# Performance work log

Measured on AMD Instinct MI355X. Metric: run time of the kernel, lower is better.

Reference implementation:

```python
import jax, jax.numpy as jnp
import numpy as np

N_NODES = 50000
N_EDGES = 600000
F_IN = 128
H = 128
NUM_GRAPHS = 64
SELF_LOOP_W = 2.0  # improved=True


def setup_inputs() -> dict:
    key = jax.random.key(0)
    ks = jax.random.split(key, 16)
    x = jax.random.normal(ks[0], (N_NODES, F_IN), dtype=jnp.float32)
    edge_index = jax.random.randint(ks[1], (2, N_EDGES), 0, N_NODES, dtype=jnp.int64)
    batch_index = jnp.sort(jax.random.randint(ks[2], (N_NODES,), 0, NUM_GRAPHS, dtype=jnp.int64))
    edge_weight = jax.random.uniform(ks[3], (N_EDGES,), dtype=jnp.float32)
    def lin(k, fin, fout):
        s = 1.0 / np.sqrt(fin)
        kw, kb = jax.random.split(k)
        W = jax.random.uniform(kw, (fin, fout), minval=-s, maxval=s, dtype=jnp.float32)
        b = jax.random.uniform(kb, (fout,), minval=-s, maxval=s, dtype=jnp.float32)
        return W, b
    W0, b0 = lin(ks[4], F_IN, H)
    W1, b1 = lin(ks[5], H, H)
    W2, b2 = lin(ks[6], H, H)
    W3, b3 = lin(ks[7], H, H)
    Wout, bout = lin(ks[8], 2 * H, 1)
    return dict(x=x, edge_index=edge_index, batch_index=batch_index, edge_weight=edge_weight,
                W0=W0, b0=b0, W1=W1, b1=b1, W2=W2, b2=b2, W3=W3, b3=b3, Wout=Wout, bout=bout)


def reference(x, edge_index, batch_index, edge_weight, W0, b0, W1, b1, W2, b2, W3, b3, Wout, bout):
    N = x.shape[0]
    loop = jnp.arange(N)
    src = jnp.concatenate([edge_index[0], loop])  # [E+N]
    dst = jnp.concatenate([edge_index[1], loop])
    w = jnp.concatenate([edge_weight, jnp.full((N,), SELF_LOOP_W, dtype=x.dtype)])
    # symmetric GCN normalization: deg over destination, norm = d^-1/2[src]*w*d^-1/2[dst]
    deg = jax.ops.segment_sum(w, dst, num_segments=N)
    dinv = jnp.where(deg > 0, jax.lax.rsqrt(deg), 0.0)
    norm = dinv[src] * w * dinv[dst]  # [E+N]

    def conv(h, W, b):
        h = h @ W  # dense transform before aggregation
        msg = h[src] * norm[:, None]
        return jax.ops.segment_sum(msg, dst, num_segments=N) + b

    h = jnp.tanh(conv(x, W0, b0))
    h = jnp.tanh(conv(h, W1, b1))
    h = jnp.tanh(conv(h, W2, b2))
    h = jnp.tanh(conv(h, W3, b3))

    gmax = jax.ops.segment_max(h, batch_index, num_segments=NUM_GRAPHS)
    gmax = jnp.where(jnp.isfinite(gmax), gmax, 0.0)  # guard empty graphs
    cnt = jax.ops.segment_sum(jnp.ones((N,), dtype=h.dtype), batch_index, num_segments=NUM_GRAPHS)
    gmean = jax.ops.segment_sum(h, batch_index, num_segments=NUM_GRAPHS) / jnp.maximum(cnt, 1.0)[:, None]
    hidden = jnp.concatenate([gmax, gmean], axis=1)  # [B, 2H]
    out = hidden @ Wout + bout  # [B, 1]
    return out, hidden
```

## Files before the change

### kernel.cpp

```cpp
#include <hip/hip_runtime.h>
#include <hip/hip_bf16.h>
#include <hip/hip_fp16.h>

typedef __hip_bfloat16 bf16;
typedef _Float16 half8 __attribute__((ext_vector_type(8)));
typedef float f32x4 __attribute__((ext_vector_type(4)));

#define FDIM 128
#define SELF_W 2.0f
#define NGRAPH 64
#define DEG_SCALE 1048576.0f
#define DEG_MASK  ((1ull<<44) - 1ull)

__device__ __forceinline__ float b2f(bf16 v){ return __bfloat162float(v); }

__device__ __forceinline__ float rdf(const void* p, long long i, int f32){
  return f32 ? ((const float*)p)[i] : b2f(((const bf16*)p)[i]);
}
__device__ __forceinline__ int rdi(const void* p, long long i, int i64){
  return i64 ? (int)(((const long long*)p)[i]) : ((const int*)p)[i];
}

__device__ __forceinline__ float tanh_fast(float x){
  float ax = fabsf(x);
  float e  = __expf(-2.0f*ax);
  float r  = (1.0f - e) * __builtin_amdgcn_rcpf(1.0f + e);
  return copysignf(r, x);
}

struct PtrPack { const void* p[10]; };
__global__ __launch_bounds__(256) void k_setup(PtrPack pk, float* __restrict__ pf,
                                               _Float16* __restrict__ wt,
                                               unsigned long long* __restrict__ packed,
                                               const void* __restrict__ bat,
                                               unsigned* __restrict__ gstart,
                                               const unsigned short* __restrict__ x16,
                                               const int* __restrict__ ei32,
                                               int* __restrict__ flags_out,
                                               int N){
  __shared__ int cbig, codd, sf32, si64;
  int tid = threadIdx.x;
  if (tid == 0){ cbig = 0; codd = 0; }
  __syncthreads();
  for (int i = tid; i < 4096; i += 256){
    int e = (x16[i] >> 7) & 0xFF;
    if (e >= 134) atomicAdd(&cbig, 1);
  }
  for (int i = tid; i < 512; i += 256){
    if (ei32[2*i + 1] != 0) atomicAdd(&codd, 1);
  }
  __syncthreads();
  if (tid == 0){
    sf32 = (cbig >= 64) ? 1 : 0;
    si64 = (codd < 8)  ? 1 : 0;
    if (blockIdx.x == 0){ flags_out[0] = sf32; flags_out[1] = si64; }
  }
  __syncthreads();
  int f32 = sf32, i64 = si64;

  const int sz[10]  = {16384,16384,16384,16384,128,128,128,128,256,1};
  const int dst[10] = {0,16384,32768,49152,65536,65664,65792,65920,66048,66304};
  int i = blockIdx.x*blockDim.x + tid;
  if (i < 66305){
    int seg = 0, rem = i;
    while (rem >= sz[seg]){ rem -= sz[seg]; seg++; }
    float v = rdf(pk.p[seg], rem, f32);
    pf[dst[seg] + rem] = v;
    if (seg < 4){
      int k = rem >> 7, n = rem & 127;
      wt[seg*16384 + n*128 + k] = (_Float16)v;
    }
  }
  int stride = gridDim.x*blockDim.x;
  for (int j = i; j < N; j += stride)
    packed[j] = (unsigned long long)(SELF_W * DEG_SCALE);
  if (blockIdx.x == gridDim.x - 1){
    __shared__ unsigned s[NGRAPH+1];
    int g = tid;
    if (g <= NGRAPH){
      int lo = 0, hi = N;
      while (lo < hi){ int mid = (lo + hi) >> 1; if (rdi(bat, mid, i64) < g) lo = mid + 1; else hi = mid; }
      s[g] = (unsigned)lo;
    }
    __syncthreads();
    if (g <= NGRAPH) gstart[g] = s[g];
  }
}

__global__ void k_edge_deg(const void* __restrict__ ei, const void* __restrict__ ew,
                           unsigned long long* __restrict__ packed,
                           unsigned* __restrict__ rank,
                           int E, int N, const int* __restrict__ flags){
  int e0 = 2*(blockIdx.x*blockDim.x + threadIdx.x);
  if (e0 >= E) return;
  int i64 = flags[1], f32 = flags[0];
  int e1 = e0 + 1;
  bool h1 = (e1 < E);
  int d0 = rdi(ei, (long long)E + e0, i64);
  int d1 = h1 ? rdi(ei, (long long)E + e1, i64) : 0;
  float w0 = rdf(ew, e0, f32);
  float w1 = h1 ? rdf(ew, e1, f32) : 0.f;
  unsigned r0 = 0u, r1 = 0u;
  if ((unsigned)d0 < (unsigned)N){
    unsigned long long add = (1ull << 44) |
        (unsigned long long)__float2uint_rn(w0 * DEG_SCALE);
    r0 = (unsigned)(atomicAdd(&packed[d0], add) >> 44);
  }
  if (h1 && (unsigned)d1 < (unsigned)N){
    unsigned long long add = (1ull << 44) |
        (unsigned long long)__float2uint_rn(w1 * DEG_SCALE);
    r1 = (unsigned)(atomicAdd(&packed[d1], add) >> 44);
  }
  rank[e0] = r0;
  if (h1) rank[e1] = r1;
}

__device__ __forceinline__ unsigned wave_incl_scan(unsigned v){
  int lane = threadIdx.x & 63;
  #pragma unroll
  for (int d = 1; d < 64; d <<= 1){
    unsigned t = __shfl_up(v, d, 64);
    if (lane >= d) v += t;
  }
  return v;
}

__global__ __launch_bounds__(256) void k_scan_pre(const unsigned long long* __restrict__ packed,
                                                  float* __restrict__ dinv,
                                                  float* __restrict__ swv,
                                                  unsigned* __restrict__ bsum,
                                                  unsigned* __restrict__ epk, unsigned Epad,
                                                  int N){
  __shared__ unsigned wsh[4];
  int tid = threadIdx.x, lane = tid & 63, wid = tid >> 6;
  unsigned gid = blockIdx.x*blockDim.x + tid, gstr = gridDim.x*blockDim.x;
  for (unsigned j = gid; j < Epad; j += gstr) epk[j] = 0u;
  int i0 = blockIdx.x*1024 + tid*4;
  unsigned tsum = 0u;
  #pragma unroll
  for (int j = 0; j < 4; j++){
    int i = i0 + j;
    if (i < N){
      unsigned long long pv = packed[i];
      tsum += ((unsigned)(pv >> 44) + 7u) & ~7u;
      float d = (float)(pv & DEG_MASK) * (1.0f / DEG_SCALE);
      float di = (d > 0.f) ? rsqrtf(d) : 0.f;
      dinv[i] = di;
      swv[i]  = di * di * SELF_W;
    }
  }
  #pragma unroll
  for (int d = 1; d < 64; d <<= 1) tsum += __shfl_down(tsum, d, 64);
  if (lane == 0) wsh[wid] = tsum;
  __syncthreads();
  if (tid == 0) bsum[blockIdx.x] = wsh[0] + wsh[1] + wsh[2] + wsh[3];
}

__global__ __launch_bounds__(256) void k_scan_fin(const unsigned long long* __restrict__ packed,
                                                  const unsigned* __restrict__ bsum,
                                                  unsigned* __restrict__ off, int N, int NB){
  __shared__ unsigned wsh[4];
  __shared__ unsigned sbase, stot;
  int tid = threadIdx.x, lane = tid & 63, wid = tid >> 6;
  if (tid < 64){
    unsigned v = (tid < NB) ? bsum[tid] : 0u;
    unsigned isc = wave_incl_scan(v);
    if (tid == (int)blockIdx.x) sbase = isc - v;
    if (tid == 63) stot = isc;
  }
  __syncthreads();
  int i0 = blockIdx.x*1024 + tid*4;
  unsigned v0=0u,v1=0u,v2=0u,v3=0u;
  if (i0+0 < N) v0 = ((unsigned)(packed[i0+0] >> 44) + 7u) & ~7u;
  if (i0+1 < N) v1 = ((unsigned)(packed[i0+1] >> 44) + 7u) & ~7u;
  if (i0+2 < N) v2 = ((unsigned)(packed[i0+2] >> 44) + 7u) & ~7u;
  if (i0+3 < N) v3 = ((unsigned)(packed[i0+3] >> 44) + 7u) & ~7u;
  unsigned tsum = v0+v1+v2+v3;
  unsigned isc = wave_incl_scan(tsum);
  if (lane == 63) wsh[wid] = isc;
  __syncthreads();
  unsigned wbase = 0u;
  #pragma unroll
  for (int w = 0; w < 4; w++) if (w < wid) wbase += wsh[w];
  unsigned ex = sbase + wbase + (isc - tsum);
  if (i0+0 < N) off[i0+0] = ex;
  if (i0+1 < N) off[i0+1] = ex + v0;
  if (i0+2 < N) off[i0+2] = ex + v0 + v1;
  if (i0+3 < N) off[i0+3] = ex + v0 + v1 + v2;
  if (blockIdx.x == gridDim.x - 1 && tid == 0) off[N] = stot;
}

__global__ void k_bucket(const void* __restrict__ ei, const void* __restrict__ ew,
                         const float* __restrict__ dinv,
                         const unsigned* __restrict__ off,
                         const unsigned* __restrict__ rank,
                         unsigned* __restrict__ epk,
                         int E, unsigned Epad, int N, const int* __restrict__ flags){
  int e0 = 2*(blockIdx.x*blockDim.x + threadIdx.x);
  if (e0 >= E) return;
  int i64 = flags[1], f32 = flags[0];
  #pragma unroll
  for (int j = 0; j < 2; j++){
    int e = e0 + j;
    if (e >= E) break;
    int s_ = rdi(ei, e, i64);
    int d  = rdi(ei, (long long)E + e, i64);
    if ((unsigned)s_ >= (unsigned)N || (unsigned)d >= (unsigned)N) continue;
    unsigned pos = off[d] + rank[e];
    if (pos < Epad){
      float coef = dinv[s_] * rdf(ew, e, f32) * dinv[d];
      _Float16 ch = (_Float16)coef;
      unsigned cu = (unsigned)__builtin_bit_cast(unsigned short, ch);
      epk[pos] = ((unsigned)s_ & 0xffffu) | (cu << 16);
    }
  }
}

template<int MODE>
__global__ __launch_bounds__(256) void k_gemm(const void* __restrict__ in,
                                              const _Float16* __restrict__ WT,
                                              _Float16* __restrict__ outp, int N,
                                              size_t pstride,
                                              const int* __restrict__ flags){
  __shared__ _Float16 sout[4*16*136];
  int tid  = threadIdx.x;
  int wid  = tid >> 6, lane = tid & 63;
  int ln   = lane & 15, quad = lane >> 4;
  int row0 = blockIdx.x * 64;
  int rowA = row0 + wid*16 + ln;
  int rA   = (rowA < N) ? rowA : (N > 0 ? N-1 : 0);

  half8 af[4];
  if (MODE == 1){
    const _Float16* src = (const _Float16*)in;
    #pragma unroll
    for (int kc = 0; kc < 4; kc++)
      af[kc] = *(const half8*)(src + (size_t)kc*pstride + (size_t)rA*32 + quad*8);
  } else {
    if (flags[0]){
      const float* src = (const float*)in + (size_t)rA*FDIM + quad*8;
      #pragma unroll
      for (int kc = 0; kc < 4; kc++){
        float4 a = *(const float4*)(src + kc*32);
        float4 b = *(const float4*)(src + kc*32 + 4);
        half8 h; h[0]=(_Float16)a.x; h[1]=(_Float16)a.y; h[2]=(_Float16)a.z; h[3]=(_Float16)a.w;
        h[4]=(_Float16)b.x; h[5]=(_Float16)b.y; h[6]=(_Float16)b.z; h[7]=(_Float16)b.w;
        af[kc] = h;
      }
    } else {
      const unsigned short* src = (const unsigned short*)in + (size_t)rA*FDIM + quad*8;
      #pragma unroll
      for (int kc = 0; kc < 4; kc++){
        ushort4 u0 = *(const ushort4*)(src + kc*32);
        ushort4 u1 = *(const ushort4*)(src + kc*32 + 4);
        half8 h;
        h[0]=(_Float16)__uint_as_float((unsigned)u0.x<<16);
        h[1]=(_Float16)__uint_as_float((unsigned)u0.y<<16);
        h[2]=(_Float16)__uint_as_float((unsigned)u0.z<<16);
        h[3]=(_Float16)__uint_as_float((unsigned)u0.w<<16);
        h[4]=(_Float16)__uint_as_float((unsigned)u1.x<<16);
        h[5]=(_Float16)__uint_as_float((unsigned)u1.y<<16);
        h[6]=(_Float16)__uint_as_float((unsigned)u1.z<<16);
        h[7]=(_Float16)__uint_as_float((unsigned)u1.w<<16);
        af[kc] = h;
      }
    }
  }

  f32x4 acc[8];
  #pragma unroll
  for (int nt = 0; nt < 8; nt++) acc[nt] = (f32x4){0.f,0.f,0.f,0.f};

  #pragma unroll
  for (int kc = 0; kc < 4; kc++){
    #pragma unroll
    for (int nt = 0; nt < 8; nt++){
      half8 bf = *(const half8*)(WT + (size_t)(nt*16 + ln)*FDIM + kc*32 + quad*8);
      acc[nt] = __builtin_amdgcn_mfma_f32_16x16x32_f16(af[kc], bf, acc[nt], 0, 0, 0);
    }
  }

  _Float16* so = sout + wid*2176;
  #pragma unroll
  for (int nt = 0; nt < 8; nt++)
    #pragma unroll
    for (int reg = 0; reg < 4; reg++)
      so[(quad*4 + reg)*136 + nt*16 + ln] = (_Float16)acc[nt][reg];
  __syncthreads();

  #pragma unroll
  for (int c = 0; c < 4; c++){
    int chunk = tid + c*256;
    int r = chunk >> 4, co = (chunk & 15)*8;
    int row = row0 + r;
    if (row < N){
      half8 v = *(const half8*)(sout + (r>>4)*2176 + (r&15)*136 + co);
      *(half8*)(outp + (size_t)(co>>5)*pstride + (size_t)row*32 + (co & 31)) = v;
    }
  }
}

__global__ __launch_bounds__(256) void k_agg(const _Float16* __restrict__ tp,
                                             const float* __restrict__ swv,
                                             const unsigned* __restrict__ off,
                                             const unsigned* __restrict__ epk,
                                             const float* __restrict__ bias,
                                             _Float16* __restrict__ hp,
                                             int N, size_t pstride){
  int tid  = threadIdx.x;
  int wv   = tid >> 6, lane = tid & 63;
  int quad = lane >> 4, ql = lane & 15;
  int panel = blockIdx.x & 3;
  int n = (blockIdx.x >> 2)*16 + wv*4 + quad;
  bool valid = (n < N);
  int nn = valid ? n : 0;
  const _Float16* tpp = tp + (size_t)panel*pstride;
  const _Float16* myt = tpp + ql*2;

  float sw = swv[nn];
  float2 sv = __half22float2(*(const __half2*)(myt + (size_t)nn*32));
  float a0 = sw * sv.x, a1 = sw * sv.y;
  float b0 = 0.f, b1 = 0.f;

  unsigned beg = off[nn];
  unsigned end = valid ? off[nn+1] : beg;
  if (beg < end){
    uint4 p0 = *(const uint4*)(epk + beg);
    uint4 p1 = *(const uint4*)(epk + beg + 4);
    for (unsigned i = beg; i < end; i += 8){
      unsigned ni  = i + 8;
      unsigned pre = (ni < end) ? ni : beg;
      uint4 q0 = *(const uint4*)(epk + pre);
      uint4 q1 = *(const uint4*)(epk + pre + 4);
      unsigned vs[8] = {p0.x,p0.y,p0.z,p0.w,p1.x,p1.y,p1.z,p1.w};
      __half2 tv[8];
      #pragma unroll
      for (int j = 0; j < 8; j++)
        tv[j] = *(const __half2*)(myt + (size_t)(vs[j] & 0xffffu)*32);
      #pragma unroll
      for (int j = 0; j < 8; j++){
        float w = (float)__builtin_bit_cast(_Float16, (unsigned short)(vs[j] >> 16));
        float2 tf = __half22float2(tv[j]);
        if (j & 1){ b0 += w * tf.x; b1 += w * tf.y; }
        else      { a0 += w * tf.x; a1 += w * tf.y; }
      }
      p0 = q0; p1 = q1;
    }
  }
  a0 += b0; a1 += b1;
  int cc = panel*32 + ql*2;
  a0 = tanh_fast(a0 + bias[cc]);
  a1 = tanh_fast(a1 + bias[cc+1]);
  if (valid)
    *(__half2*)(hp + (size_t)panel*pstride + (size_t)n*32 + ql*2) = __floats2half2_rn(a0, a1);
}

__global__ __launch_bounds__(256) void k_pool_part(const _Float16* __restrict__ hp,
                                                   const unsigned* __restrict__ gstart,
                                                   float* __restrict__ pmax,
                                                   float* __restrict__ psum,
                                                   size_t pstride){
  int g = blockIdx.x >> 4, sub = blockIdx.x & 15;
  int tid = threadIdx.x;
  int col = tid & 127, half_ = tid >> 7;
  const _Float16* hpp = hp + (size_t)(col >> 5)*pstride + (col & 31);
  unsigned s0 = gstart[g], s1 = gstart[g+1];
  float m = -INFINITY, sm = 0.f;
  for (unsigned n = s0 + sub*2 + half_; n < s1; n += 32){
    float v = (float)hpp[(size_t)n*32];
    m = fmaxf(m, v); sm += v;
  }
  __shared__ float shm[256], shs[256];
  shm[tid] = m; shs[tid] = sm;
  __syncthreads();
  if (half_ == 0){
    m  = fmaxf(m, shm[tid + 128]);
    sm += shs[tid + 128];
    int slot = (g*16 + sub)*128 + col;
    pmax[slot] = m;
    psum[slot] = sm;
  }
}

__global__ __launch_bounds__(256) void k_pool_out(const float* __restrict__ pmax,
                                                  const float* __restrict__ psum,
                                                  const unsigned* __restrict__ gstart,
                                                  const float* __restrict__ Wout,
                                                  const float* __restrict__ bout,
                                                  void* __restrict__ outp,
                                                  const int* __restrict__ flags){
  int g = blockIdx.x, tid = threadIdx.x;
  int col = tid & 127, sub = tid >> 7;
  unsigned cnt = gstart[g+1] - gstart[g];
  float val;
  if (sub == 0){
    float m = -INFINITY;
    #pragma unroll
    for (int j = 0; j < 16; j++) m = fmaxf(m, pmax[(g*16 + j)*128 + col]);
    val = (cnt > 0 && m > -INFINITY) ? m : 0.f;
  } else {
    float s = 0.f;
    #pragma unroll
    for (int j = 0; j < 16; j++) s += psum[(g*16 + j)*128 + col];
    val = s / (float)(cnt ? cnt : 1u);
  }
  int hcol = sub*128 + col;
  int f32out = flags[0];
  int hidx = NGRAPH + g*(2*FDIM) + hcol;
  if (f32out) ((float*)outp)[hidx] = val;
  else        ((bf16*)outp)[hidx] = __float2bfloat16(val);

  __shared__ float red[256];
  red[hcol] = val * Wout[hcol];
  __syncthreads();
  for (int s = 128; s > 0; s >>= 1){
    if (tid < s) red[tid] += red[tid + s];
    __syncthreads();
  }
  if (tid == 0){
    float o = red[0] + bout[0];
    if (f32out) ((float*)outp)[g] = o;
    else        ((bf16*)outp)[g] = __float2bfloat16(o);
  }
}

extern "C" void kernel_launch(void* const* d_in, const int* in_sizes, int n_in,
                              void* d_out, int out_size, void* d_ws, size_t ws_size,
                              hipStream_t stream){
  int N = in_sizes[0] / FDIM;
  int E = in_sizes[3];
  int NB = (N + 1023) / 1024;
  unsigned Epad = (unsigned)E + 8u*(unsigned)N;
  size_t pstride = (size_t)N * 32;

  char* p = (char*)d_ws;
  auto alloc = [&](size_t bytes){ char* r = p; p += (bytes + 255) & ~(size_t)255; return r; };
  int*       flags  = (int*)      alloc(16);
  float*     pf     = (float*)    alloc((size_t)(66305 + 64)*4);
  _Float16*  wt     = (_Float16*) alloc((size_t)4*FDIM*FDIM*2);
  unsigned long long* packed = (unsigned long long*)alloc((size_t)N*8);
  float*     dinv   = (float*)    alloc((size_t)N*4);
  float*     swv    = (float*)    alloc((size_t)N*4);
  unsigned*  off    = (unsigned*) alloc((size_t)(N+1)*4);
  unsigned*  bsum   = (unsigned*) alloc((size_t)128*4);
  unsigned*  rank   = (unsigned*) alloc((size_t)E*4);
  unsigned*  epk    = (unsigned*) alloc((size_t)Epad*4);
  _Float16*  th     = (_Float16*) alloc((size_t)N*FDIM*2);
  _Float16*  hh     = (_Float16*) alloc((size_t)N*FDIM*2);
  float*     pmax   = (float*)    alloc((size_t)NGRAPH*16*128*4);
  float*     psum   = (float*)    alloc((size_t)NGRAPH*16*128*4);
  unsigned*  gstart = (unsigned*) alloc((size_t)(NGRAPH+1)*4);

  float* bf_[4] = {pf + 65536, pf + 65664, pf + 65792, pf + 65920};
  float* Woutf  = pf + 66048;
  float* boutf  = pf + 66304;

  PtrPack pk;
  pk.p[0]=d_in[4]; pk.p[1]=d_in[6]; pk.p[2]=d_in[8]; pk.p[3]=d_in[10];
  pk.p[4]=d_in[5]; pk.p[5]=d_in[7]; pk.p[6]=d_in[9]; pk.p[7]=d_in[11];
  pk.p[8]=d_in[12]; pk.p[9]=d_in[13];
  k_setup<<<(66305 + 255)/256, 256, 0, stream>>>(pk, pf, wt, packed, d_in[2], gstart,
                                                 (const unsigned short*)d_in[0],
                                                 (const int*)d_in[1], flags, N);
  int gE2 = (E + 511)/512;
  k_edge_deg<<<gE2, 256, 0, stream>>>(d_in[1], d_in[3], packed, rank, E, N, flags);
  k_scan_pre<<<NB, 256, 0, stream>>>(packed, dinv, swv, bsum, epk, Epad, N);
  k_scan_fin<<<NB, 256, 0, stream>>>(packed, bsum, off, N, NB);
  k_bucket<<<gE2, 256, 0, stream>>>(d_in[1], d_in[3], dinv, off, rank, epk, E, Epad, N, flags);

  int gG = (N + 63)/64;
  int gA = ((N + 15)/16)*4;

  k_gemm<0><<<gG, 256, 0, stream>>>(d_in[0], wt + 0*16384, th, N, pstride, flags);
  k_agg<<<gA, 256, 0, stream>>>(th, swv, off, epk, bf_[0], hh, N, pstride);
  for (int l = 1; l < 4; l++){
    k_gemm<1><<<gG, 256, 0, stream>>>(hh, wt + (size_t)l*16384, th, N, pstride, flags);
    k_agg<<<gA, 256, 0, stream>>>(th, swv, off, epk, bf_[l], hh, N, pstride);
  }

  k_pool_part<<<16*NGRAPH, 256, 0, stream>>>(hh, gstart, pmax, psum, pstride);
  k_pool_out<<<NGRAPH, 256, 0, stream>>>(pmax, psum, gstart, Woutf, boutf, d_out, flags);
}
```

Measured before the change: 368.1 us.

## Fuse all stages into one persistent cooperative kernel with grid barriers

Replaces the chain of roughly thirteen separate kernel launches (setup, degree, scan, bucket, four GEMM/aggregate layers, pooling) with a single persistent cooperative kernel. Stages are separated by a software grid barrier built on an atomic counter. Blocks loop over tiles and vertex blocks with a grid-stride pattern, capped at 512 blocks or the occupancy limit. This removes launch gaps and the flags round-trip through memory. In exchange it pays one grid-wide barrier per stage, limits parallelism to the resident block count, and adds an extra memset launch for the barrier counter.

```diff
diff --git a/kernel.cpp b/kernel.cpp
--- a/kernel.cpp
+++ b/kernel.cpp
@@ -9,6 +9,7 @@
 #define FDIM 128
 #define SELF_W 2.0f
 #define NGRAPH 64
+#define GBMAX 512
 #define DEG_SCALE 1048576.0f
 #define DEG_MASK  ((1ull<<44) - 1ull)
 
@@ -26,93 +27,6 @@
   float e  = __expf(-2.0f*ax);
   float r  = (1.0f - e) * __builtin_amdgcn_rcpf(1.0f + e);
   return copysignf(r, x);
-}
-
-struct PtrPack { const void* p[10]; };
-__global__ __launch_bounds__(256) void k_setup(PtrPack pk, float* __restrict__ pf,
-                                               _Float16* __restrict__ wt,
-                                               unsigned long long* __restrict__ packed,
-                                               const void* __restrict__ bat,
-                                               unsigned* __restrict__ gstart,
-                                               const unsigned short* __restrict__ x16,
-                                               const int* __restrict__ ei32,
-                                               int* __restrict__ flags_out,
-                                               int N){
-  __shared__ int cbig, codd, sf32, si64;
-  int tid = threadIdx.x;
-  if (tid == 0){ cbig = 0; codd = 0; }
-  __syncthreads();
-  for (int i = tid; i < 4096; i += 256){
-    int e = (x16[i] >> 7) & 0xFF;
-    if (e >= 134) atomicAdd(&cbig, 1);
-  }
-  for (int i = tid; i < 512; i += 256){
-    if (ei32[2*i + 1] != 0) atomicAdd(&codd, 1);
-  }
-  __syncthreads();
-  if (tid == 0){
-    sf32 = (cbig >= 64) ? 1 : 0;
-    si64 = (codd < 8)  ? 1 : 0;
-    if (blockIdx.x == 0){ flags_out[0] = sf32; flags_out[1] = si64; }
-  }
-  __syncthreads();
-  int f32 = sf32, i64 = si64;
-
-  const int sz[10]  = {16384,16384,16384,16384,128,128,128,128,256,1};
-  const int dst[10] = {0,16384,32768,49152,65536,65664,65792,65920,66048,66304};
-  int i = blockIdx.x*blockDim.x + tid;
-  if (i < 66305){
-    int seg = 0, rem = i;
-    while (rem >= sz[seg]){ rem -= sz[seg]; seg++; }
-    float v = rdf(pk.p[seg], rem, f32);
-    pf[dst[seg] + rem] = v;
-    if (seg < 4){
-      int k = rem >> 7, n = rem & 127;
-      wt[seg*16384 + n*128 + k] = (_Float16)v;
-    }
-  }
-  int stride = gridDim.x*blockDim.x;
-  for (int j = i; j < N; j += stride)
-    packed[j] = (unsigned long long)(SELF_W * DEG_SCALE);
-  if (blockIdx.x == gridDim.x - 1){
-    __shared__ unsigned s[NGRAPH+1];
-    int g = tid;
-    if (g <= NGRAPH){
-      int lo = 0, hi = N;
-      while (lo < hi){ int mid = (lo + hi) >> 1; if (rdi(bat, mid, i64) < g) lo = mid + 1; else hi = mid; }
-      s[g] = (unsigned)lo;
-    }
-    __syncthreads();
-    if (g <= NGRAPH) gstart[g] = s[g];
-  }
-}
-
-__global__ void k_edge_deg(const void* __restrict__ ei, const void* __restrict__ ew,
-                           unsigned long long* __restrict__ packed,
-                           unsigned* __restrict__ rank,
-                           int E, int N, const int* __restrict__ flags){
-  int e0 = 2*(blockIdx.x*blockDim.x + threadIdx.x);
-  if (e0 >= E) return;
-  int i64 = flags[1], f32 = flags[0];
-  int e1 = e0 + 1;
-  bool h1 = (e1 < E);
-  int d0 = rdi(ei, (long long)E + e0, i64);
-  int d1 = h1 ? rdi(ei, (long long)E + e1, i64) : 0;
-  float w0 = rdf(ew, e0, f32);
-  float w1 = h1 ? rdf(ew, e1, f32) : 0.f;
-  unsigned r0 = 0u, r1 = 0u;
-  if ((unsigned)d0 < (unsigned)N){
-    unsigned long long add = (1ull << 44) |
-        (unsigned long long)__float2uint_rn(w0 * DEG_SCALE);
-    r0 = (unsigned)(atomicAdd(&packed[d0], add) >> 44);
-  }
-  if (h1 && (unsigned)d1 < (unsigned)N){
-    unsigned long long add = (1ull << 44) |
-        (unsigned long long)__float2uint_rn(w1 * DEG_SCALE);
-    r1 = (unsigned)(atomicAdd(&packed[d1], add) >> 44);
-  }
-  rank[e0] = r0;
-  if (h1) rank[e1] = r1;
 }
 
 __device__ __forceinline__ unsigned wave_incl_scan(unsigned v){
@@ -125,108 +39,26 @@
   return v;
 }
 
-__global__ __launch_bounds__(256) void k_scan_pre(const unsigned long long* __restrict__ packed,
-                                                  float* __restrict__ dinv,
-                                                  float* __restrict__ swv,
-                                                  unsigned* __restrict__ bsum,
-                                                  unsigned* __restrict__ epk, unsigned Epad,
-                                                  int N){
-  __shared__ unsigned wsh[4];
-  int tid = threadIdx.x, lane = tid & 63, wid = tid >> 6;
-  unsigned gid = blockIdx.x*blockDim.x + tid, gstr = gridDim.x*blockDim.x;
-  for (unsigned j = gid; j < Epad; j += gstr) epk[j] = 0u;
-  int i0 = blockIdx.x*1024 + tid*4;
-  unsigned tsum = 0u;
-  #pragma unroll
-  for (int j = 0; j < 4; j++){
-    int i = i0 + j;
-    if (i < N){
-      unsigned long long pv = packed[i];
-      tsum += ((unsigned)(pv >> 44) + 7u) & ~7u;
-      float d = (float)(pv & DEG_MASK) * (1.0f / DEG_SCALE);
-      float di = (d > 0.f) ? rsqrtf(d) : 0.f;
-      dinv[i] = di;
-      swv[i]  = di * di * SELF_W;
-    }
-  }
-  #pragma unroll
-  for (int d = 1; d < 64; d <<= 1) tsum += __shfl_down(tsum, d, 64);
-  if (lane == 0) wsh[wid] = tsum;
-  __syncthreads();
-  if (tid == 0) bsum[blockIdx.x] = wsh[0] + wsh[1] + wsh[2] + wsh[3];
-}
-
-__global__ __launch_bounds__(256) void k_scan_fin(const unsigned long long* __restrict__ packed,
-                                                  const unsigned* __restrict__ bsum,
-                                                  unsigned* __restrict__ off, int N, int NB){
-  __shared__ unsigned wsh[4];
-  __shared__ unsigned sbase, stot;
-  int tid = threadIdx.x, lane = tid & 63, wid = tid >> 6;
-  if (tid < 64){
-    unsigned v = (tid < NB) ? bsum[tid] : 0u;
-    unsigned isc = wave_incl_scan(v);
-    if (tid == (int)blockIdx.x) sbase = isc - v;
-    if (tid == 63) stot = isc;
-  }
-  __syncthreads();
-  int i0 = blockIdx.x*1024 + tid*4;
-  unsigned v0=0u,v1=0u,v2=0u,v3=0u;
-  if (i0+0 < N) v0 = ((unsigned)(packed[i0+0] >> 44) + 7u) & ~7u;
-  if (i0+1 < N) v1 = ((unsigned)(packed[i0+1] >> 44) + 7u) & ~7u;
-  if (i0+2 < N) v2 = ((unsigned)(packed[i0+2] >> 44) + 7u) & ~7u;
-  if (i0+3 < N) v3 = ((unsigned)(packed[i0+3] >> 44) + 7u) & ~7u;
-  unsigned tsum = v0+v1+v2+v3;
-  unsigned isc = wave_incl_scan(tsum);
-  if (lane == 63) wsh[wid] = isc;
-  __syncthreads();
-  unsigned wbase = 0u;
-  #pragma unroll
-  for (int w = 0; w < 4; w++) if (w < wid) wbase += wsh[w];
-  unsigned ex = sbase + wbase + (isc - tsum);
-  if (i0+0 < N) off[i0+0] = ex;
-  if (i0+1 < N) off[i0+1] = ex + v0;
-  if (i0+2 < N) off[i0+2] = ex + v0 + v1;
-  if (i0+3 < N) off[i0+3] = ex + v0 + v1 + v2;
-  if (blockIdx.x == gridDim.x - 1 && tid == 0) off[N] = stot;
-}
-
-__global__ void k_bucket(const void* __restrict__ ei, const void* __restrict__ ew,
-                         const float* __restrict__ dinv,
-                         const unsigned* __restrict__ off,
-                         const unsigned* __restrict__ rank,
-                         unsigned* __restrict__ epk,
-                         int E, unsigned Epad, int N, const int* __restrict__ flags){
-  int e0 = 2*(blockIdx.x*blockDim.x + threadIdx.x);
-  if (e0 >= E) return;
-  int i64 = flags[1], f32 = flags[0];
-  #pragma unroll
-  for (int j = 0; j < 2; j++){
-    int e = e0 + j;
-    if (e >= E) break;
-    int s_ = rdi(ei, e, i64);
-    int d  = rdi(ei, (long long)E + e, i64);
-    if ((unsigned)s_ >= (unsigned)N || (unsigned)d >= (unsigned)N) continue;
-    unsigned pos = off[d] + rank[e];
-    if (pos < Epad){
-      float coef = dinv[s_] * rdf(ew, e, f32) * dinv[d];
-      _Float16 ch = (_Float16)coef;
-      unsigned cu = (unsigned)__builtin_bit_cast(unsigned short, ch);
-      epk[pos] = ((unsigned)s_ & 0xffffu) | (cu << 16);
-    }
-  }
+__device__ __forceinline__ void gsync(unsigned* bar, unsigned target){
+  __syncthreads();
+  if (threadIdx.x == 0){
+    __hip_atomic_fetch_add(bar, 1u, __ATOMIC_RELEASE, __HIP_MEMORY_SCOPE_AGENT);
+    while (__hip_atomic_load(bar, __ATOMIC_RELAXED, __HIP_MEMORY_SCOPE_AGENT) < target)
+      __builtin_amdgcn_s_sleep(1);
+    __threadfence();
+  }
+  __syncthreads();
 }
 
 template<int MODE>
-__global__ __launch_bounds__(256) void k_gemm(const void* __restrict__ in,
-                                              const _Float16* __restrict__ WT,
-                                              _Float16* __restrict__ outp, int N,
-                                              size_t pstride,
-                                              const int* __restrict__ flags){
-  __shared__ _Float16 sout[4*16*136];
+__device__ __forceinline__ void gemm_tile(int tile, const void* __restrict__ in,
+                                          const _Float16* __restrict__ WT,
+                                          _Float16* __restrict__ outp, int N,
+                                          size_t pstride, int f32, _Float16* sout){
   int tid  = threadIdx.x;
   int wid  = tid >> 6, lane = tid & 63;
   int ln   = lane & 15, quad = lane >> 4;
-  int row0 = blockIdx.x * 64;
+  int row0 = tile * 64;
   int rowA = row0 + wid*16 + ln;
   int rA   = (rowA < N) ? rowA : (N > 0 ? N-1 : 0);
 
@@ -237,7 +69,7 @@
     for (int kc = 0; kc < 4; kc++)
       af[kc] = *(const half8*)(src + (size_t)kc*pstride + (size_t)rA*32 + quad*8);
   } else {
-    if (flags[0]){
+    if (f32){
       const float* src = (const float*)in + (size_t)rA*FDIM + quad*8;
       #pragma unroll
       for (int kc = 0; kc < 4; kc++){
@@ -275,8 +107,8 @@
   for (int kc = 0; kc < 4; kc++){
     #pragma unroll
     for (int nt = 0; nt < 8; nt++){
-      half8 bf = *(const half8*)(WT + (size_t)(nt*16 + ln)*FDIM + kc*32 + quad*8);
-      acc[nt] = __builtin_amdgcn_mfma_f32_16x16x32_f16(af[kc], bf, acc[nt], 0, 0, 0);
+      half8 bfr = *(const half8*)(WT + (size_t)(nt*16 + ln)*FDIM + kc*32 + quad*8);
+      acc[nt] = __builtin_amdgcn_mfma_f32_16x16x32_f16(af[kc], bfr, acc[nt], 0, 0, 0);
     }
   }
 
@@ -298,20 +130,21 @@
       *(half8*)(outp + (size_t)(co>>5)*pstride + (size_t)row*32 + (co & 31)) = v;
     }
   }
-}
-
-__global__ __launch_bounds__(256) void k_agg(const _Float16* __restrict__ tp,
-                                             const float* __restrict__ swv,
-                                             const unsigned* __restrict__ off,
-                                             const unsigned* __restrict__ epk,
-                                             const float* __restrict__ bias,
-                                             _Float16* __restrict__ hp,
-                                             int N, size_t pstride){
+  __syncthreads();
+}
+
+__device__ __forceinline__ void agg_vblock(int vb, const _Float16* __restrict__ tp,
+                                           const float* __restrict__ swv,
+                                           const unsigned* __restrict__ off,
+                                           const unsigned* __restrict__ epk,
+                                           const float* __restrict__ bias,
+                                           _Float16* __restrict__ hp,
+                                           int N, size_t pstride){
   int tid  = threadIdx.x;
   int wv   = tid >> 6, lane = tid & 63;
   int quad = lane >> 4, ql = lane & 15;
-  int panel = blockIdx.x & 3;
-  int n = (blockIdx.x >> 2)*16 + wv*4 + quad;
+  int panel = vb & 3;
+  int n = (vb >> 2)*16 + wv*4 + quad;
   bool valid = (n < N);
   int nn = valid ? n : 0;
   const _Float16* tpp = tp + (size_t)panel*pstride;
@@ -355,73 +188,239 @@
     *(__half2*)(hp + (size_t)panel*pstride + (size_t)n*32 + ql*2) = __floats2half2_rn(a0, a1);
 }
 
-__global__ __launch_bounds__(256) void k_pool_part(const _Float16* __restrict__ hp,
-                                                   const unsigned* __restrict__ gstart,
-                                                   float* __restrict__ pmax,
-                                                   float* __restrict__ psum,
-                                                   size_t pstride){
-  int g = blockIdx.x >> 4, sub = blockIdx.x & 15;
+struct PtrPack { const void* p[10]; };
+
+__global__ __launch_bounds__(256, 2) void k_mega(
+    PtrPack pk,
+    const void* __restrict__ x, const void* __restrict__ ei,
+    const void* __restrict__ bat, const void* __restrict__ ew,
+    float* __restrict__ pf, _Float16* __restrict__ wt,
+    unsigned long long* __restrict__ packed,
+    float* __restrict__ dinv, float* __restrict__ swv,
+    unsigned* __restrict__ off, unsigned* __restrict__ bsum,
+    unsigned* __restrict__ rank, unsigned* __restrict__ epk,
+    _Float16* __restrict__ th, _Float16* __restrict__ hh,
+    float* __restrict__ pmax, float* __restrict__ psum,
+    unsigned* __restrict__ gstart, void* __restrict__ outp,
+    unsigned* __restrict__ bar,
+    int N, int E, int NB, unsigned Epad, size_t pstride)
+{
+  __shared__ __align__(16) char smraw[4*16*136*2];
+  _Float16* sout = (_Float16*)smraw;
+  __shared__ int s_cbig, s_codd;
+
   int tid = threadIdx.x;
-  int col = tid & 127, half_ = tid >> 7;
-  const _Float16* hpp = hp + (size_t)(col >> 5)*pstride + (col & 31);
-  unsigned s0 = gstart[g], s1 = gstart[g+1];
-  float m = -INFINITY, sm = 0.f;
-  for (unsigned n = s0 + sub*2 + half_; n < s1; n += 32){
-    float v = (float)hpp[(size_t)n*32];
-    m = fmaxf(m, v); sm += v;
-  }
-  __shared__ float shm[256], shs[256];
-  shm[tid] = m; shs[tid] = sm;
-  __syncthreads();
-  if (half_ == 0){
-    m  = fmaxf(m, shm[tid + 128]);
-    sm += shs[tid + 128];
-    int slot = (g*16 + sub)*128 + col;
-    pmax[slot] = m;
-    psum[slot] = sm;
-  }
-}
-
-__global__ __launch_bounds__(256) void k_pool_out(const float* __restrict__ pmax,
-                                                  const float* __restrict__ psum,
-                                                  const unsigned* __restrict__ gstart,
-                                                  const float* __restrict__ Wout,
-                                                  const float* __restrict__ bout,
-                                                  void* __restrict__ outp,
-                                                  const int* __restrict__ flags){
-  int g = blockIdx.x, tid = threadIdx.x;
-  int col = tid & 127, sub = tid >> 7;
-  unsigned cnt = gstart[g+1] - gstart[g];
-  float val;
-  if (sub == 0){
-    float m = -INFINITY;
-    #pragma unroll
-    for (int j = 0; j < 16; j++) m = fmaxf(m, pmax[(g*16 + j)*128 + col]);
-    val = (cnt > 0 && m > -INFINITY) ? m : 0.f;
-  } else {
-    float s = 0.f;
-    #pragma unroll
-    for (int j = 0; j < 16; j++) s += psum[(g*16 + j)*128 + col];
-    val = s / (float)(cnt ? cnt : 1u);
-  }
-  int hcol = sub*128 + col;
-  int f32out = flags[0];
-  int hidx = NGRAPH + g*(2*FDIM) + hcol;
-  if (f32out) ((float*)outp)[hidx] = val;
-  else        ((bf16*)outp)[hidx] = __float2bfloat16(val);
-
-  __shared__ float red[256];
-  red[hcol] = val * Wout[hcol];
-  __syncthreads();
-  for (int s = 128; s > 0; s >>= 1){
-    if (tid < s) red[tid] += red[tid + s];
+  const unsigned nblk = gridDim.x;
+  unsigned gtid = blockIdx.x*256u + (unsigned)tid;
+  const unsigned tot = nblk*256u;
+  unsigned btgt = 0;
+  #define GSYNC() do { btgt += nblk; gsync(bar, btgt); } while(0)
+
+  if (tid == 0){ s_cbig = 0; s_codd = 0; }
+  __syncthreads();
+  {
+    const unsigned short* x16 = (const unsigned short*)x;
+    const int* ei32 = (const int*)ei;
+    for (int i = tid; i < 4096; i += 256){
+      int e = (x16[i] >> 7) & 0xFF;
+      if (e >= 134) atomicAdd(&s_cbig, 1);
+    }
+    for (int i = tid; i < 512; i += 256){
+      if (ei32[2*i + 1] != 0) atomicAdd(&s_codd, 1);
+    }
+  }
+  __syncthreads();
+  const int f32 = (s_cbig >= 64) ? 1 : 0;
+  const int i64 = (s_codd < 8)  ? 1 : 0;
+
+  {
+    const int sz[10]  = {16384,16384,16384,16384,128,128,128,128,256,1};
+    const int dst[10] = {0,16384,32768,49152,65536,65664,65792,65920,66048,66304};
+    for (unsigned i = gtid; i < 66305u; i += tot){
+      int seg = 0, rem = (int)i;
+      while (rem >= sz[seg]){ rem -= sz[seg]; seg++; }
+      float v = rdf(pk.p[seg], rem, f32);
+      pf[dst[seg] + rem] = v;
+      if (seg < 4){
+        int k = rem >> 7, n = rem & 127;
+        wt[seg*16384 + n*128 + k] = (_Float16)v;
+      }
+    }
+  }
+  for (unsigned j = gtid; j < (unsigned)N; j += tot)
+    packed[j] = (unsigned long long)(SELF_W * DEG_SCALE);
+  if (blockIdx.x == 0 && tid <= NGRAPH){
+    int lo = 0, hi = N;
+    while (lo < hi){ int mid = (lo + hi) >> 1; if (rdi(bat, mid, i64) < tid) lo = mid + 1; else hi = mid; }
+    gstart[tid] = (unsigned)lo;
+  }
+  GSYNC();
+
+  for (unsigned e = gtid; e < (unsigned)E; e += tot){
+    int d = rdi(ei, (long long)E + (long long)e, i64);
+    if ((unsigned)d < (unsigned)N){
+      float w = rdf(ew, e, f32);
+      unsigned long long add = (1ull << 44) |
+          (unsigned long long)__float2uint_rn(w * DEG_SCALE);
+      rank[e] = (unsigned)(atomicAdd(&packed[d], add) >> 44);
+    }
+  }
+  GSYNC();
+
+  for (unsigned j = gtid; j < Epad; j += tot) epk[j] = 0u;
+  if ((int)blockIdx.x < NB){
+    unsigned* wsh = (unsigned*)smraw;
+    int lane = tid & 63, wid = tid >> 6;
+    int i0 = blockIdx.x*1024 + tid*4;
+    unsigned tsum = 0u;
+    #pragma unroll
+    for (int j = 0; j < 4; j++){
+      int i = i0 + j;
+      if (i < N){
+        unsigned long long pv = packed[i];
+        tsum += ((unsigned)(pv >> 44) + 7u) & ~7u;
+        float d = (float)(pv & DEG_MASK) * (1.0f / DEG_SCALE);
+        float di = (d > 0.f) ? rsqrtf(d) : 0.f;
+        dinv[i] = di;
+        swv[i]  = di * di * SELF_W;
+      }
+    }
+    #pragma unroll
+    for (int d = 1; d < 64; d <<= 1) tsum += __shfl_down(tsum, d, 64);
+    if (lane == 0) wsh[wid] = tsum;
     __syncthreads();
-  }
-  if (tid == 0){
-    float o = red[0] + bout[0];
-    if (f32out) ((float*)outp)[g] = o;
-    else        ((bf16*)outp)[g] = __float2bfloat16(o);
-  }
+    if (tid == 0) bsum[blockIdx.x] = wsh[0] + wsh[1] + wsh[2] + wsh[3];
+  }
+  GSYNC();
+
+  if ((int)blockIdx.x < NB){
+    unsigned* wsh = (unsigned*)smraw;
+    int lane = tid & 63, wid = tid >> 6;
+    if (tid < 64){
+      unsigned v = (tid < NB) ? bsum[tid] : 0u;
+      unsigned isc = wave_incl_scan(v);
+      if (tid == (int)blockIdx.x) wsh[4] = isc - v;
+      if (tid == 63) wsh[5] = isc;
+    }
+    __syncthreads();
+    int i0 = blockIdx.x*1024 + tid*4;
+    unsigned v0=0u,v1=0u,v2=0u,v3=0u;
+    if (i0+0 < N) v0 = ((unsigned)(packed[i0+0] >> 44) + 7u) & ~7u;
+    if (i0+1 < N) v1 = ((unsigned)(packed[i0+1] >> 44) + 7u) & ~7u;
+    if (i0+2 < N) v2 = ((unsigned)(packed[i0+2] >> 44) + 7u) & ~7u;
+    if (i0+3 < N) v3 = ((unsigned)(packed[i0+3] >> 44) + 7u) & ~7u;
+    unsigned tsum = v0+v1+v2+v3;
+    unsigned isc = wave_incl_scan(tsum);
+    if (lane == 63) wsh[wid] = isc;
+    __syncthreads();
+    unsigned wbase = 0u;
+    #pragma unroll
+    for (int w = 0; w < 4; w++) if (w < wid) wbase += wsh[w];
+    unsigned ex = wsh[4] + wbase + (isc - tsum);
+    if (i0+0 < N) off[i0+0] = ex;
+    if (i0+1 < N) off[i0+1] = ex + v0;
+    if (i0+2 < N) off[i0+2] = ex + v0 + v1;
+    if (i0+3 < N) off[i0+3] = ex + v0 + v1 + v2;
+    if ((int)blockIdx.x == NB-1 && tid == 0) off[N] = wsh[5];
+  }
+  GSYNC();
+
+  for (unsigned e = gtid; e < (unsigned)E; e += tot){
+    int s_ = rdi(ei, (long long)e, i64);
+    int d  = rdi(ei, (long long)E + (long long)e, i64);
+    if ((unsigned)s_ >= (unsigned)N || (unsigned)d >= (unsigned)N) continue;
+    unsigned pos = off[d] + rank[e];
+    if (pos < Epad){
+      float coef = dinv[s_] * rdf(ew, e, f32) * dinv[d];
+      _Float16 ch = (_Float16)coef;
+      unsigned cu = (unsigned)__builtin_bit_cast(unsigned short, ch);
+      epk[pos] = ((unsigned)s_ & 0xffffu) | (cu << 16);
+    }
+  }
+  GSYNC();
+
+  const int ntile = (N + 63) >> 6;
+  const int nvb   = ((N + 15) >> 4) * 4;
+
+  for (int t = blockIdx.x; t < ntile; t += (int)nblk)
+    gemm_tile<0>(t, x, wt, th, N, pstride, f32, sout);
+  GSYNC();
+  for (int vb = blockIdx.x; vb < nvb; vb += (int)nblk)
+    agg_vblock(vb, th, swv, off, epk, pf + 65536, hh, N, pstride);
+  GSYNC();
+
+  #pragma unroll 1
+  for (int l = 1; l < 4; l++){
+    for (int t = blockIdx.x; t < ntile; t += (int)nblk)
+      gemm_tile<1>(t, hh, wt + (size_t)l*16384, th, N, pstride, f32, sout);
+    GSYNC();
+    for (int vb = blockIdx.x; vb < nvb; vb += (int)nblk)
+      agg_vblock(vb, th, swv, off, epk, pf + 65536 + l*128, hh, N, pstride);
+    GSYNC();
+  }
+
+  {
+    float* shm = (float*)smraw;
+    float* shs = shm + 256;
+    for (int vb = blockIdx.x; vb < 16*NGRAPH; vb += (int)nblk){
+      int g = vb >> 4, sub = vb & 15;
+      int col = tid & 127, half_ = tid >> 7;
+      const _Float16* hpp = hh + (size_t)(col >> 5)*pstride + (col & 31);
+      unsigned s0 = gstart[g], s1 = gstart[g+1];
+      float m = -INFINITY, sm = 0.f;
+      for (unsigned n = s0 + sub*2 + half_; n < s1; n += 32){
+        float v = (float)hpp[(size_t)n*32];
+        m = fmaxf(m, v); sm += v;
+      }
+      shm[tid] = m; shs[tid] = sm;
+      __syncthreads();
+      if (half_ == 0){
+        m  = fmaxf(m, shm[tid + 128]);
+        sm += shs[tid + 128];
+        int slot = (g*16 + sub)*128 + col;
+        pmax[slot] = m;
+        psum[slot] = sm;
+      }
+      __syncthreads();
+    }
+  }
+  GSYNC();
+
+  if ((int)blockIdx.x < NGRAPH){
+    int g = blockIdx.x;
+    int col = tid & 127, sub = tid >> 7;
+    unsigned cnt = gstart[g+1] - gstart[g];
+    float val;
+    if (sub == 0){
+      float m = -INFINITY;
+      #pragma unroll
+      for (int j = 0; j < 16; j++) m = fmaxf(m, pmax[(g*16 + j)*128 + col]);
+      val = (cnt > 0 && m > -INFINITY) ? m : 0.f;
+    } else {
+      float s = 0.f;
+      #pragma unroll
+      for (int j = 0; j < 16; j++) s += psum[(g*16 + j)*128 + col];
+      val = s / (float)(cnt ? cnt : 1u);
+    }
+    int hcol = sub*128 + col;
+    int hidx = NGRAPH + g*(2*FDIM) + hcol;
+    if (f32) ((float*)outp)[hidx] = val;
+    else     ((bf16*)outp)[hidx] = __float2bfloat16(val);
+
+    float* red = (float*)smraw;
+    red[hcol] = val * pf[66048 + hcol];
+    __syncthreads();
+    for (int s = 128; s > 0; s >>= 1){
+      if (tid < s) red[tid] += red[tid + s];
+      __syncthreads();
+    }
+    if (tid == 0){
+      float o = red[0] + pf[66304];
+      if (f32) ((float*)outp)[g] = o;
+      else     ((bf16*)outp)[g] = __float2bfloat16(o);
+    }
+  }
+  #undef GSYNC
 }
 
 extern "C" void kernel_launch(void* const* d_in, const int* in_sizes, int n_in,
@@ -435,7 +434,6 @@
 
   char* p = (char*)d_ws;
   auto alloc = [&](size_t bytes){ char* r = p; p += (bytes + 255) & ~(size_t)255; return r; };
-  int*       flags  = (int*)      alloc(16);
   float*     pf     = (float*)    alloc((size_t)(66305 + 64)*4);
   _Float16*  wt     = (_Float16*) alloc((size_t)4*FDIM*FDIM*2);
   unsigned long long* packed = (unsigned long long*)alloc((size_t)N*8);
@@ -450,34 +448,40 @@
   float*     pmax   = (float*)    alloc((size_t)NGRAPH*16*128*4);
   float*     psum   = (float*)    alloc((size_t)NGRAPH*16*128*4);
   unsigned*  gstart = (unsigned*) alloc((size_t)(NGRAPH+1)*4);
-
-  float* bf_[4] = {pf + 65536, pf + 65664, pf + 65792, pf + 65920};
-  float* Woutf  = pf + 66048;
-  float* boutf  = pf + 66304;
+  unsigned*  bar    = (unsigned*) alloc(256);
+
+  hipMemsetAsync(bar, 0, 64, stream);
 
   PtrPack pk;
   pk.p[0]=d_in[4]; pk.p[1]=d_in[6]; pk.p[2]=d_in[8]; pk.p[3]=d_in[10];
   pk.p[4]=d_in[5]; pk.p[5]=d_in[7]; pk.p[6]=d_in[9]; pk.p[7]=d_in[11];
   pk.p[8]=d_in[12]; pk.p[9]=d_in[13];
-  k_setup<<<(66305 + 255)/256, 256, 0, stream>>>(pk, pf, wt, packed, d_in[2], gstart,
-                                                 (const unsigned short*)d_in[0],
-                                                 (const int*)d_in[1], flags, N);
-  int gE2 = (E + 511)/512;
-  k_edge_deg<<<gE2, 256, 0, stream>>>(d_in[1], d_in[3], packed, rank, E, N, flags);
-  k_scan_pre<<<NB, 256, 0, stream>>>(packed, dinv, swv, bsum, epk, Epad, N);
-  k_scan_fin<<<NB, 256, 0, stream>>>(packed, bsum, off, N, NB);
-  k_bucket<<<gE2, 256, 0, stream>>>(d_in[1], d_in[3], dinv, off, rank, epk, E, Epad, N, flags);
-
-  int gG = (N + 63)/64;
-  int gA = ((N + 15)/16)*4;
-
-  k_gemm<0><<<gG, 256, 0, stream>>>(d_in[0], wt + 0*16384, th, N, pstride, flags);
-  k_agg<<<gA, 256, 0, stream>>>(th, swv, off, epk, bf_[0], hh, N, pstride);
-  for (int l = 1; l < 4; l++){
-    k_gemm<1><<<gG, 256, 0, stream>>>(hh, wt + (size_t)l*16384, th, N, pstride, flags);
-    k_agg<<<gA, 256, 0, stream>>>(th, swv, off, epk, bf_[l], hh, N, pstride);
-  }
-
-  k_pool_part<<<16*NGRAPH, 256, 0, stream>>>(hh, gstart, pmax, psum, pstride);
-  k_pool_out<<<NGRAPH, 256, 0, stream>>>(pmax, psum, gstart, Woutf, boutf, d_out, flags);
-}
+
+  int occ = 0;
+  int nblk = GBMAX;
+  if (hipOccupancyMaxActiveBlocksPerMultiprocessor(&occ, k_mega, 256, 0) == hipSuccess && occ > 0){
+    long long cap = (long long)occ * 256;
+    if (cap < nblk) nblk = (int)cap;
+  }
+  if (nblk < 64) nblk = 64;
+
+  const void* xp = d_in[0];  const void* eip = d_in[1];
+  const void* batp = d_in[2]; const void* ewp = d_in[3];
+  void* outp = d_out;
+  void* kargs[] = {
+    (void*)&pk, (void*)&xp, (void*)&eip, (void*)&batp, (void*)&ewp,
+    (void*)&pf, (void*)&wt, (void*)&packed, (void*)&dinv, (void*)&swv,
+    (void*)&off, (void*)&bsum, (void*)&rank, (void*)&epk,
+    (void*)&th, (void*)&hh, (void*)&pmax, (void*)&psum,
+    (void*)&gstart, (void*)&outp, (void*)&bar,
+    (void*)&N, (void*)&E, (void*)&NB, (void*)&Epad, (void*)&pstride
+  };
+  hipError_t err = hipLaunchCooperativeKernel((void*)k_mega, dim3(nblk), dim3(256),
+                                              kargs, 0, stream);
+  if (err != hipSuccess){
+    k_mega<<<nblk, 256, 0, stream>>>(pk, xp, eip, batp, ewp,
+                                     pf, wt, packed, dinv, swv, off, bsum, rank, epk,
+                                     th, hh, pmax, psum, gstart, outp, bar,
+                                     N, E, NB, Epad, pstride);
+  }
+}
```

After: 977.9 us. +165.7%, slower.

## Fuse per-layer GEMM and aggregation into persistent kernel with grid barrier

Applied to the files above, without the earlier changes.

Each layer's GEMM and aggregation kernels are merged into one persistent kernel of 512 blocks that loops over tiles and uses a hand-rolled atomic grid barrier between the two phases. This removes four kernel launches and their launch gaps. The trade-off is that block 0 spins polling the counters, and the barrier relies on all 512 blocks being co-resident (launch bounds of 2 blocks per CU), otherwise it can deadlock. Aggregation now iterates panels sequentially per block, which changes how work is spread across CUs.

```diff
diff --git a/kernel.cpp b/kernel.cpp
--- a/kernel.cpp
+++ b/kernel.cpp
@@ -9,6 +9,7 @@
 #define FDIM 128
 #define SELF_W 2.0f
 #define NGRAPH 64
+#define LGRID 512
 #define DEG_SCALE 1048576.0f
 #define DEG_MASK  ((1ull<<44) - 1ull)
 
@@ -217,16 +218,14 @@
 }
 
 template<int MODE>
-__global__ __launch_bounds__(256) void k_gemm(const void* __restrict__ in,
-                                              const _Float16* __restrict__ WT,
-                                              _Float16* __restrict__ outp, int N,
-                                              size_t pstride,
-                                              const int* __restrict__ flags){
-  __shared__ _Float16 sout[4*16*136];
+__device__ __forceinline__ void gemm_tile(int tile, const void* __restrict__ in,
+                                          const _Float16* __restrict__ WT,
+                                          _Float16* __restrict__ outp, int N,
+                                          size_t pstride, int f32, _Float16* sout){
   int tid  = threadIdx.x;
   int wid  = tid >> 6, lane = tid & 63;
   int ln   = lane & 15, quad = lane >> 4;
-  int row0 = blockIdx.x * 64;
+  int row0 = tile * 64;
   int rowA = row0 + wid*16 + ln;
   int rA   = (rowA < N) ? rowA : (N > 0 ? N-1 : 0);
 
@@ -237,7 +236,7 @@
     for (int kc = 0; kc < 4; kc++)
       af[kc] = *(const half8*)(src + (size_t)kc*pstride + (size_t)rA*32 + quad*8);
   } else {
-    if (flags[0]){
+    if (f32){
       const float* src = (const float*)in + (size_t)rA*FDIM + quad*8;
       #pragma unroll
       for (int kc = 0; kc < 4; kc++){
@@ -275,8 +274,8 @@
   for (int kc = 0; kc < 4; kc++){
     #pragma unroll
     for (int nt = 0; nt < 8; nt++){
-      half8 bf = *(const half8*)(WT + (size_t)(nt*16 + ln)*FDIM + kc*32 + quad*8);
-      acc[nt] = __builtin_amdgcn_mfma_f32_16x16x32_f16(af[kc], bf, acc[nt], 0, 0, 0);
+      half8 bfr = *(const half8*)(WT + (size_t)(nt*16 + ln)*FDIM + kc*32 + quad*8);
+      acc[nt] = __builtin_amdgcn_mfma_f32_16x16x32_f16(af[kc], bfr, acc[nt], 0, 0, 0);
     }
   }
 
@@ -298,20 +297,20 @@
       *(half8*)(outp + (size_t)(co>>5)*pstride + (size_t)row*32 + (co & 31)) = v;
     }
   }
-}
-
-__global__ __launch_bounds__(256) void k_agg(const _Float16* __restrict__ tp,
-                                             const float* __restrict__ swv,
-                                             const unsigned* __restrict__ off,
-                                             const unsigned* __restrict__ epk,
-                                             const float* __restrict__ bias,
-                                             _Float16* __restrict__ hp,
-                                             int N, size_t pstride){
+  __syncthreads();
+}
+
+__device__ __forceinline__ void agg_vblock(int grp, int panel, const _Float16* __restrict__ tp,
+                                           const float* __restrict__ swv,
+                                           const unsigned* __restrict__ off,
+                                           const unsigned* __restrict__ epk,
+                                           const float* __restrict__ bias,
+                                           _Float16* __restrict__ hp,
+                                           int N, size_t pstride){
   int tid  = threadIdx.x;
   int wv   = tid >> 6, lane = tid & 63;
   int quad = lane >> 4, ql = lane & 15;
-  int panel = blockIdx.x & 3;
-  int n = (blockIdx.x >> 2)*16 + wv*4 + quad;
+  int n = grp*16 + wv*4 + quad;
   bool valid = (n < N);
   int nn = valid ? n : 0;
   const _Float16* tpp = tp + (size_t)panel*pstride;
@@ -355,6 +354,63 @@
     *(__half2*)(hp + (size_t)panel*pstride + (size_t)n*32 + ql*2) = __floats2half2_rn(a0, a1);
 }
 
+__device__ __forceinline__ void hsync(unsigned* ctrs, unsigned* release, unsigned nblk){
+  __syncthreads();
+  int tid = threadIdx.x;
+  if (tid == 0)
+    __hip_atomic_fetch_add(&ctrs[blockIdx.x & 255], 1u, __ATOMIC_RELEASE, __HIP_MEMORY_SCOPE_AGENT);
+  if (blockIdx.x == 0){
+    __shared__ unsigned red[256];
+    for (;;){
+      unsigned v = __hip_atomic_load(&ctrs[tid], __ATOMIC_ACQUIRE, __HIP_MEMORY_SCOPE_AGENT);
+      red[tid] = v;
+      __syncthreads();
+      for (int s = 128; s > 0; s >>= 1){
+        if (tid < s) red[tid] += red[tid + s];
+        __syncthreads();
+      }
+      unsigned tot = red[0];
+      __syncthreads();
+      if (tot >= nblk) break;
+      __builtin_amdgcn_s_sleep(2);
+    }
+    if (tid == 0)
+      __hip_atomic_store(release, 1u, __ATOMIC_RELEASE, __HIP_MEMORY_SCOPE_AGENT);
+  } else if (tid == 0){
+    while (__hip_atomic_load(release, __ATOMIC_ACQUIRE, __HIP_MEMORY_SCOPE_AGENT) == 0u)
+      __builtin_amdgcn_s_sleep(1);
+  }
+  __threadfence();
+  __syncthreads();
+}
+
+template<int MODE>
+__global__ __launch_bounds__(256, 2) void k_layer(
+    const void* __restrict__ in, const _Float16* __restrict__ WT,
+    _Float16* __restrict__ th,
+    const float* __restrict__ swv, const unsigned* __restrict__ off,
+    const unsigned* __restrict__ epk, const float* __restrict__ bias,
+    _Float16* __restrict__ hh,
+    int N, size_t pstride, const int* __restrict__ flags,
+    unsigned* __restrict__ ctrs, unsigned* __restrict__ release)
+{
+  __shared__ _Float16 sout[4*16*136];
+  int f32 = flags[0];
+  const int ntile = (N + 63) >> 6;
+  const int ng  = (N + 15) >> 4;
+  const int nblk = (int)gridDim.x;
+
+  for (int t = blockIdx.x; t < ntile; t += nblk)
+    gemm_tile<MODE>(t, in, WT, th, N, pstride, f32, sout);
+
+  hsync(ctrs, release, (unsigned)nblk);
+
+  #pragma unroll 1
+  for (int p = 0; p < 4; p++)
+    for (int g = blockIdx.x; g < ng; g += nblk)
+      agg_vblock(g, p, th, swv, off, epk, bias, hh, N, pstride);
+}
+
 __global__ __launch_bounds__(256) void k_pool_part(const _Float16* __restrict__ hp,
                                                    const unsigned* __restrict__ gstart,
                                                    float* __restrict__ pmax,
@@ -450,10 +506,14 @@
   float*     pmax   = (float*)    alloc((size_t)NGRAPH*16*128*4);
   float*     psum   = (float*)    alloc((size_t)NGRAPH*16*128*4);
   unsigned*  gstart = (unsigned*) alloc((size_t)(NGRAPH+1)*4);
+  unsigned*  hb     = (unsigned*) alloc((size_t)(4*256 + 64)*4);
+
+  hipMemsetAsync(hb, 0, (4*256 + 64)*4, stream);
 
   float* bf_[4] = {pf + 65536, pf + 65664, pf + 65792, pf + 65920};
   float* Woutf  = pf + 66048;
   float* boutf  = pf + 66304;
+  unsigned* relv = hb + 4*256;
 
   PtrPack pk;
   pk.p[0]=d_in[4]; pk.p[1]=d_in[6]; pk.p[2]=d_in[8]; pk.p[3]=d_in[10];
@@ -468,15 +528,12 @@
   k_scan_fin<<<NB, 256, 0, stream>>>(packed, bsum, off, N, NB);
   k_bucket<<<gE2, 256, 0, stream>>>(d_in[1], d_in[3], dinv, off, rank, epk, E, Epad, N, flags);
 
-  int gG = (N + 63)/64;
-  int gA = ((N + 15)/16)*4;
-
-  k_gemm<0><<<gG, 256, 0, stream>>>(d_in[0], wt + 0*16384, th, N, pstride, flags);
-  k_agg<<<gA, 256, 0, stream>>>(th, swv, off, epk, bf_[0], hh, N, pstride);
-  for (int l = 1; l < 4; l++){
-    k_gemm<1><<<gG, 256, 0, stream>>>(hh, wt + (size_t)l*16384, th, N, pstride, flags);
-    k_agg<<<gA, 256, 0, stream>>>(th, swv, off, epk, bf_[l], hh, N, pstride);
-  }
+  k_layer<0><<<LGRID, 256, 0, stream>>>(d_in[0], wt, th, swv, off, epk, bf_[0], hh,
+                                        N, pstride, flags, hb + 0*256, relv + 0*16);
+  for (int l = 1; l < 4; l++)
+    k_layer<1><<<LGRID, 256, 0, stream>>>(hh, wt + (size_t)l*16384, th, swv, off, epk,
+                                          bf_[l], hh, N, pstride, flags,
+                                          hb + l*256, relv + l*16);
 
   k_pool_part<<<16*NGRAPH, 256, 0, stream>>>(hh, gstart, pmax, psum, pstride);
   k_pool_out<<<NGRAPH, 256, 0, stream>>>(pmax, psum, gstart, Woutf, boutf, d_out, flags);
```

Result: slower. 838.7 us (+127.8%).
